# Performance work log

Hardware: AMD Instinct MI355X
Metric: run time of the kernel (lower is better)

## Reference

```python
import jax, jax.numpy as jnp
import numpy as np

NUM_HEADS = 16
WINDOW = 256  # window_size: each query i attends to keys [max(0, i-W+1), i]


def setup_inputs() -> dict:
    key = jax.random.key(0)
    k1, k2, k3, k4, k5 = jax.random.split(key, 5)
    B, S, D = 2, 4096, 1024
    scale = 0.02
    return {
        "x": jax.random.normal(k1, (B, S, D), dtype=jnp.float32),
        "wq": jax.random.normal(k2, (D, D), dtype=jnp.float32) * scale,
        "wk": jax.random.normal(k3, (D, D), dtype=jnp.float32) * scale,
        "wv": jax.random.normal(k4, (D, D), dtype=jnp.float32) * scale,
        "wo": jax.random.normal(k5, (D, D), dtype=jnp.float32) * scale,
    }


def _sliding_window_attn(x, wq, wk, wv, wo):
    B, S, D = x.shape
    H, W = NUM_HEADS, WINDOW
    Dh = D // H
    nb = S // W  # number of query blocks (S assumed divisible by W)

    def proj(w):
        # nn.Linear: y = x @ w.T ; -> [B, H, nb, W, Dh]
        y = (x @ w.T).reshape(B, nb, W, H, Dh)
        return y.transpose(0, 3, 1, 2, 4)

    q = proj(wq)
    k = proj(wk)
    v = proj(wv)

    # Each query block j attends to key blocks j-1 and j (banded causal window).
    zpad = jnp.zeros((B, H, 1, W, Dh), dtype=x.dtype)
    kpad = jnp.concatenate([zpad, k], axis=2)  # [B,H,nb+1,W,Dh]
    vpad = jnp.concatenate([zpad, v], axis=2)
    k2 = jnp.concatenate([kpad[:, :, :-1], kpad[:, :, 1:]], axis=3)  # [B,H,nb,2W,Dh]
    v2 = jnp.concatenate([vpad[:, :, :-1], vpad[:, :, 1:]], axis=3)

    scores = jnp.einsum("bhjqd,bhjkd->bhjqk", q, k2) / jnp.sqrt(
        jnp.asarray(Dh, dtype=x.dtype)
    )  # [B,H,nb,W,2W]

    # Mask: query global pos i = j*W + qi; key global pos kp = (j-1)*W + ki.
    # Valid iff i-W+1 <= kp <= i  <=>  qi+1 <= ki <= qi+W ; and kp >= 0.
    qi = jnp.arange(W)[:, None]          # [W,1]
    ki = jnp.arange(2 * W)[None, :]      # [1,2W]
    band = (ki >= qi + 1) & (ki <= qi + W)                      # [W,2W]
    kpos_ok = (jnp.arange(nb)[:, None, None] - 1) * W + ki[None] >= 0  # [nb,1,2W]
    mask = band[None] & kpos_ok          # [nb,W,2W]

    neg = jnp.finfo(scores.dtype).min
    scores = jnp.where(mask[None, None], scores, neg)
    attn = jax.nn.softmax(scores, axis=-1)

    out = jnp.einsum("bhjqk,bhjkd->bhjqd", attn, v2)  # [B,H,nb,W,Dh]
    out = out.transpose(0, 2, 3, 1, 4).reshape(B, S, D)
    return out @ wo.T


def reference(x, wq, wk, wv, wo):
    return _sliding_window_attn(x, wq, wk, wv, wo)
```

## Files before the change

kernel.cpp:

```cpp
#include <hip/hip_runtime.h>

#define S_LEN 4096
#define DMODEL 1024
#define NH 16
#define DH 64
#define WIN 256
#define NQKV 3072

typedef __attribute__((ext_vector_type(8))) short short8;
typedef __attribute__((ext_vector_type(4))) short sh4;
typedef __attribute__((ext_vector_type(4))) float floatx4;

__device__ __forceinline__ ushort f2bf(float f) {
    union { float f; unsigned int i; } x;
    x.f = f;
    unsigned int r = x.i + 0x7FFFu + ((x.i >> 16) & 1u);
    return (ushort)(r >> 16);
}

__global__ __launch_bounds__(256) void cvt_all(const float* __restrict__ x,
                                               const float* __restrict__ wq,
                                               const float* __restrict__ wk,
                                               const float* __restrict__ wv,
                                               const float* __restrict__ wo,
                                               ushort* __restrict__ xb,
                                               ushort* __restrict__ W3b,
                                               ushort* __restrict__ wob,
                                               int nx8, int nw8) {
    int i = blockIdx.x * 256 + threadIdx.x;
    const float* src;
    ushort* dst;
    if (i < nx8) {
        src = x + (size_t)i * 8;            dst = xb + (size_t)i * 8;
    } else {
        int j = i - nx8;
        int which = j / nw8, r = j - which * nw8;
        if (which >= 4) return;
        const float* w4[4] = {wq, wk, wv, wo};
        src = w4[which] + (size_t)r * 8;
        dst = (which == 3 ? wob : W3b + (size_t)which * nw8 * 8) + (size_t)r * 8;
    }
    floatx4 f0 = *(const floatx4*)src;
    floatx4 f1 = *(const floatx4*)(src + 4);
    short8 v;
#pragma unroll
    for (int e = 0; e < 4; ++e) v[e] = (short)f2bf(f0[e]);
#pragma unroll
    for (int e = 0; e < 4; ++e) v[4 + e] = (short)f2bf(f1[e]);
    *(short8*)dst = v;
}

#define GLOAD16(src, dst)                                                     \
    __builtin_amdgcn_global_load_lds(                                         \
        (const __attribute__((address_space(1))) void*)(src),                 \
        (__attribute__((address_space(3))) void*)(dst), 16, 0, 0)

template <bool OUTF32>
__global__ __launch_bounds__(256, 2) void gemm128(const ushort* __restrict__ A,
                                                  const ushort* __restrict__ W,
                                                  void* __restrict__ Cout,
                                                  int M, int N, int K) {
    __shared__ __align__(16) ushort As[128 * 64];
    __shared__ __align__(16) ushort Ws[256 * 64];

    const int tid = threadIdx.x;
    const int w = tid >> 6, l = tid & 63;

    int bx, by;
    {
        const int nbx = gridDim.x, nby = gridDim.y;
        if ((nby & 7) == 0) {
            const int lin = blockIdx.y * nbx + blockIdx.x;
            const int rpb = nby >> 3;
            const int xcd = lin & 7, idx = lin >> 3;
            bx = idx / rpb;
            by = xcd * rpb + (idx - bx * rpb);
        } else {
            bx = blockIdx.x;
            by = blockIdx.y;
        }
    }
    const int bm0 = by * 128, bn0 = bx * 256;
    const int wm = (w >> 1) * 64, wn = (w & 1) * 128;
    const int lm = l & 15, quad = l >> 4;

    floatx4 acc[4][8] = {};

    int arow[4], acol[4];
#pragma unroll
    for (int p = 0; p < 4; ++p) {
        int c = p * 256 + tid;
        arow[p] = c >> 3;
        acol[p] = (((c & 7) ^ (arow[p] & 7))) * 8;
    }
    int wrow[8], wcol[8];
#pragma unroll
    for (int p = 0; p < 8; ++p) {
        int c = p * 256 + tid;
        wrow[p] = c >> 3;
        wcol[p] = (((c & 7) ^ (wrow[p] & 7))) * 8;
    }

    for (int k0 = 0; k0 < K; k0 += 64) {
#pragma unroll
        for (int p = 0; p < 4; ++p)
            GLOAD16(A + (size_t)(bm0 + arow[p]) * K + k0 + acol[p],
                    As + p * 2048 + tid * 8);
#pragma unroll
        for (int p = 0; p < 8; ++p)
            GLOAD16(W + (size_t)(bn0 + wrow[p]) * K + k0 + wcol[p],
                    Ws + p * 2048 + tid * 8);
        __syncthreads();

#pragma unroll
        for (int kk = 0; kk < 2; ++kk) {
            const int sseg = ((kk * 4 + quad) ^ (lm & 7)) * 8;
            short8 af[4], wf[8];
#pragma unroll
            for (int mi = 0; mi < 4; ++mi)
                af[mi] = *(const short8*)&As[(wm + mi * 16 + lm) * 64 + sseg];
#pragma unroll
            for (int ni = 0; ni < 8; ++ni)
                wf[ni] = *(const short8*)&Ws[(wn + ni * 16 + lm) * 64 + sseg];
#pragma unroll
            for (int mi = 0; mi < 4; ++mi)
#pragma unroll
                for (int ni = 0; ni < 8; ++ni)
                    acc[mi][ni] = __builtin_amdgcn_mfma_f32_16x16x32_bf16(
                        af[mi], wf[ni], acc[mi][ni], 0, 0, 0);
        }
        __syncthreads();
    }

#pragma unroll
    for (int mi = 0; mi < 4; ++mi)
#pragma unroll
        for (int ni = 0; ni < 8; ++ni)
#pragma unroll
            for (int r = 0; r < 4; ++r) {
                int row = bm0 + wm + mi * 16 + quad * 4 + r;
                int col = bn0 + wn + ni * 16 + lm;
                if constexpr (OUTF32)
                    ((float*)Cout)[(size_t)row * N + col] = acc[mi][ni][r];
                else
                    ((ushort*)Cout)[(size_t)row * N + col] = f2bf(acc[mi][ni][r]);
            }
}

#define KSP 72
#define VTP 136
#define PSP 40

__global__ __launch_bounds__(256) void swattn_mfma(const ushort* __restrict__ QKV,
                                                   ushort* __restrict__ O) {
    __shared__ __align__(16) ushort Ks[128 * KSP];
    __shared__ __align__(16) ushort Vt[64 * VTP];
    __shared__ __align__(16) ushort Ps[2][4 * 64 * PSP];
    __shared__ __align__(16) float lW[256];

    const int j = blockIdx.x, h = blockIdx.y, b = blockIdx.z;
    const int tid = threadIdx.x;
    const int w = tid >> 6, l = tid & 63;
    const int quad = l >> 4, lc = l & 15;

    const size_t base = (size_t)b * S_LEN * NQKV + (size_t)h * DH;
    const ushort* Qp = QKV + base;
    const ushort* Kp = QKV + base + DMODEL;
    const ushort* Vp = QKV + base + 2 * DMODEL;

    short8 qf[4][2];
#pragma unroll
    for (int nq = 0; nq < 4; ++nq)
#pragma unroll
        for (int kk = 0; kk < 2; ++kk)
            qf[nq][kk] = *(const short8*)(Qp +
                (size_t)(j * 256 + w * 64 + nq * 16 + lc) * NQKV + kk * 32 + quad * 8);

    floatx4 o[4][4] = {};
    float lsum[4] = {0.f, 0.f, 0.f, 0.f};

    const float sscale = 0.18033688011112042f;
    const float M0 = 2.0f;
    const int qlo = w * 64, qhi = w * 64 + 63;

    int skey[4], sseg[4];
#pragma unroll
    for (int i = 0; i < 4; ++i) {
        int cc = i * 256 + tid;
        skey[i] = cc >> 3;
        sseg[i] = cc & 7;
    }

    short8 kreg[4], vreg[4];
    const int c0 = (j == 0) ? 2 : 0;
    {
        const int kg0 = (j - 1) * 256 + c0 * 128;
#pragma unroll
        for (int i = 0; i < 4; ++i) {
            kreg[i] = *(const short8*)(Kp + (size_t)(kg0 + skey[i]) * NQKV + sseg[i] * 8);
            vreg[i] = *(const short8*)(Vp + (size_t)(kg0 + skey[i]) * NQKV + sseg[i] * 8);
        }
    }

    for (int c = c0; c < 4; ++c) {
        __syncthreads();
#pragma unroll
        for (int i = 0; i < 4; ++i) {
            *(short8*)&Ks[skey[i] * KSP + sseg[i] * 8] = kreg[i];
#pragma unroll
            for (int e = 0; e < 8; ++e)
                Vt[(e * 8 + sseg[i]) * VTP + skey[i]] = (ushort)vreg[i][e];
        }
        __syncthreads();

        if (c < 3) {
            const int kg0n = (j - 1) * 256 + (c + 1) * 128;
#pragma unroll
            for (int i = 0; i < 4; ++i) {
                kreg[i] = *(const short8*)(Kp + (size_t)(kg0n + skey[i]) * NQKV + sseg[i] * 8);
                vreg[i] = *(const short8*)(Vp + (size_t)(kg0n + skey[i]) * NQKV + sseg[i] * 8);
            }
        }

        const int krel0 = c * 128 - 256;
#pragma unroll
        for (int g = 0; g < 4; ++g) {
            const int k0 = krel0 + g * 32;
            if (k0 > qhi || k0 + 31 < qlo - 255) continue;
            ushort* Pw = &Ps[g & 1][w * 64 * PSP];

            floatx4 st[2][4];
            const floatx4 zero = {};
#pragma unroll
            for (int kt = 0; kt < 2; ++kt) {
                short8 kf0 = *(const short8*)&Ks[(g * 32 + kt * 16 + lc) * KSP + quad * 8];
                short8 kf1 = *(const short8*)&Ks[(g * 32 + kt * 16 + lc) * KSP + 32 + quad * 8];
#pragma unroll
                for (int nq = 0; nq < 4; ++nq) {
                    int kmin = k0 + kt * 16, qmin = qlo + nq * 16;
                    if (kmin > qmin + 15 || kmin + 270 < qmin) {
                        st[kt][nq] = zero;
                        continue;
                    }
                    st[kt][nq] = __builtin_amdgcn_mfma_f32_16x16x32_bf16(kf0, qf[nq][0], zero, 0, 0, 0);
                    st[kt][nq] = __builtin_amdgcn_mfma_f32_16x16x32_bf16(kf1, qf[nq][1], st[kt][nq], 0, 0, 0);
                }
            }
#pragma unroll
            for (int kt = 0; kt < 2; ++kt)
#pragma unroll
                for (int nq = 0; nq < 4; ++nq) {
                    sh4 pv;
                    int kmin = k0 + kt * 16, qmin = qlo + nq * 16;
                    if (kmin > qmin + 15 || kmin + 270 < qmin) {
                        pv[0] = pv[1] = pv[2] = pv[3] = 0;
                    } else if (kmin + 15 <= qmin && kmin + 240 >= qmin) {
#pragma unroll
                        for (int r = 0; r < 4; ++r) {
                            float p = exp2f(st[kt][nq][r] * sscale - M0);
                            lsum[nq] += p;
                            pv[r] = (short)f2bf(p);
                        }
                    } else {
#pragma unroll
                        for (int r = 0; r < 4; ++r) {
                            int krel = kmin + quad * 4 + r;
                            int qrel = qmin + lc;
                            bool valid = (krel <= qrel) && (krel + 255 >= qrel);
                            float p = valid ? exp2f(st[kt][nq][r] * sscale - M0) : 0.f;
                            lsum[nq] += p;
                            pv[r] = (short)f2bf(p);
                        }
                    }
                    *(sh4*)&Pw[(nq * 16 + lc) * PSP + kt * 16 + quad * 4] = pv;
                }
            __threadfence_block();

            short8 vf[4];
#pragma unroll
            for (int nd = 0; nd < 4; ++nd) {
                int prow = (lc & 7) * 8 + nd * 2 + (lc >> 3);
                vf[nd] = *(const short8*)&Vt[prow * VTP + g * 32 + quad * 8];
            }
#pragma unroll
            for (int mq = 0; mq < 4; ++mq) {
                int qmin = qlo + mq * 16;
                if (k0 > qmin + 15 || k0 + 286 < qmin) continue;
                short8 pf = *(const short8*)&Pw[(mq * 16 + lc) * PSP + quad * 8];
#pragma unroll
                for (int nd = 0; nd < 4; ++nd)
                    o[mq][nd] = __builtin_amdgcn_mfma_f32_16x16x32_bf16(pf, vf[nd], o[mq][nd], 0, 0, 0);
            }
        }
    }

#pragma unroll
    for (int nq = 0; nq < 4; ++nq) {
        lsum[nq] += __shfl_xor(lsum[nq], 16);
        lsum[nq] += __shfl_xor(lsum[nq], 32);
    }
    if (l < 16) {
#pragma unroll
        for (int nq = 0; nq < 4; ++nq) lW[w * 64 + nq * 16 + l] = lsum[nq];
    }
    __threadfence_block();
#pragma unroll
    for (int mq = 0; mq < 4; ++mq) {
        floatx4 lv = *(const floatx4*)&lW[w * 64 + mq * 16 + quad * 4];
#pragma unroll
        for (int r = 0; r < 4; ++r) {
            float inv = 1.f / lv[r];
            int token = j * 256 + w * 64 + mq * 16 + quad * 4 + r;
#pragma unroll
            for (int nd = 0; nd < 4; ++nd)
                O[(size_t)b * S_LEN * DMODEL + (size_t)token * DMODEL + h * DH + nd * 16 + lc] =
                    f2bf(o[mq][nd][r] * inv);
        }
    }
}

extern "C" void kernel_launch(void* const* d_in, const int* in_sizes, int n_in,
                              void* d_out, int out_size, void* d_ws, size_t ws_size,
                              hipStream_t stream) {
    const float* x  = (const float*)d_in[0];
    const float* wq = (const float*)d_in[1];
    const float* wk = (const float*)d_in[2];
    const float* wv = (const float*)d_in[3];
    const float* wo = (const float*)d_in[4];
    float* out = (float*)d_out;

    const int D = DMODEL;
    const int M = in_sizes[0] / D;
    const int Bb = M / S_LEN;

    ushort* xb   = (ushort*)d_ws;
    ushort* W3b  = xb + (size_t)M * D;
    ushort* wob  = W3b + (size_t)NQKV * D;
    ushort* QKVb = wob + (size_t)D * D;
    ushort* Ob   = xb;

    const int nx8 = M * D / 8, nw8 = D * D / 8;
    const int ntot = nx8 + 4 * nw8;
    cvt_all<<<dim3((ntot + 255) / 256), dim3(256), 0, stream>>>(
        x, wq, wk, wv, wo, xb, W3b, wob, nx8, nw8);

    gemm128<false><<<dim3(NQKV / 256, M / 128), dim3(256), 0, stream>>>(
        xb, W3b, QKVb, M, NQKV, D);

    swattn_mfma<<<dim3(S_LEN / WIN, NH, Bb), dim3(256), 0, stream>>>(QKVb, Ob);

    gemm128<true><<<dim3(D / 256, M / 128), dim3(256), 0, stream>>>(
        Ob, wob, out, M, D, D);
}
```

Before: 226.1 us.

## Keep softmax probabilities in registers as MFMA operand, permute V layout to match

Drops the per-wave LDS staging buffer for the probability tile: the exp results stay in the score accumulators and are packed to bf16 with v_cvt_pk_bf16_f32, then fed straight into the PV MFMA as the A operand. To make the register layout of the transposed score fragment line up with the K dimension of the PV MFMA, the key columns of the transposed V tile in LDS are permuted when stored. This removes LDS writes, reads and a block fence per 32-key group and frees shared memory, but relies on the custom permutation exactly matching the MFMA register layout and uses inline asm with truncation-vs-rounding differences.

```diff
diff --git a/kernel.cpp b/kernel.cpp
--- a/kernel.cpp
+++ b/kernel.cpp
@@ -149,13 +149,11 @@
 
 #define KSP 72
 #define VTP 136
-#define PSP 40
 
 __global__ __launch_bounds__(256) void swattn_mfma(const ushort* __restrict__ QKV,
                                                    ushort* __restrict__ O) {
     __shared__ __align__(16) ushort Ks[128 * KSP];
     __shared__ __align__(16) ushort Vt[64 * VTP];
-    __shared__ __align__(16) ushort Ps[2][4 * 64 * PSP];
     __shared__ __align__(16) float lW[256];
 
     const int j = blockIdx.x, h = blockIdx.y, b = blockIdx.z;
@@ -183,12 +181,14 @@
     const float M0 = 2.0f;
     const int qlo = w * 64, qhi = w * 64 + 63;
 
-    int skey[4], sseg[4];
+    int skey[4], sseg[4], svcol[4];
 #pragma unroll
     for (int i = 0; i < 4; ++i) {
         int cc = i * 256 + tid;
         skey[i] = cc >> 3;
         sseg[i] = cc & 7;
+        int k = skey[i];
+        svcol[i] = (k & 96) + ((k >> 2) & 3) * 8 + ((k >> 4) & 1) * 4 + (k & 3);
     }
 
     short8 kreg[4], vreg[4];
@@ -209,7 +209,7 @@
             *(short8*)&Ks[skey[i] * KSP + sseg[i] * 8] = kreg[i];
 #pragma unroll
             for (int e = 0; e < 8; ++e)
-                Vt[(e * 8 + sseg[i]) * VTP + skey[i]] = (ushort)vreg[i][e];
+                Vt[(e * 8 + sseg[i]) * VTP + svcol[i]] = (ushort)vreg[i][e];
         }
         __syncthreads();
 
@@ -227,7 +227,6 @@
         for (int g = 0; g < 4; ++g) {
             const int k0 = krel0 + g * 32;
             if (k0 > qhi || k0 + 31 < qlo - 255) continue;
-            ushort* Pw = &Ps[g & 1][w * 64 * PSP];
 
             floatx4 st[2][4];
             const floatx4 zero = {};
@@ -250,16 +249,15 @@
             for (int kt = 0; kt < 2; ++kt)
 #pragma unroll
                 for (int nq = 0; nq < 4; ++nq) {
-                    sh4 pv;
                     int kmin = k0 + kt * 16, qmin = qlo + nq * 16;
                     if (kmin > qmin + 15 || kmin + 270 < qmin) {
-                        pv[0] = pv[1] = pv[2] = pv[3] = 0;
+                        st[kt][nq] = zero;
                     } else if (kmin + 15 <= qmin && kmin + 240 >= qmin) {
 #pragma unroll
                         for (int r = 0; r < 4; ++r) {
                             float p = exp2f(st[kt][nq][r] * sscale - M0);
                             lsum[nq] += p;
-                            pv[r] = (short)f2bf(p);
+                            st[kt][nq][r] = p;
                         }
                     } else {
 #pragma unroll
@@ -269,12 +267,10 @@
                             bool valid = (krel <= qrel) && (krel + 255 >= qrel);
                             float p = valid ? exp2f(st[kt][nq][r] * sscale - M0) : 0.f;
                             lsum[nq] += p;
-                            pv[r] = (short)f2bf(p);
+                            st[kt][nq][r] = p;
                         }
                     }
-                    *(sh4*)&Pw[(nq * 16 + lc) * PSP + kt * 16 + quad * 4] = pv;
                 }
-            __threadfence_block();
 
             short8 vf[4];
 #pragma unroll
@@ -286,10 +282,18 @@
             for (int mq = 0; mq < 4; ++mq) {
                 int qmin = qlo + mq * 16;
                 if (k0 > qmin + 15 || k0 + 286 < qmin) continue;
-                short8 pf = *(const short8*)&Pw[(mq * 16 + lc) * PSP + quad * 8];
+                union { unsigned int u[4]; short8 s; } pk;
+                asm("v_cvt_pk_bf16_f32 %0, %1, %2"
+                    : "=v"(pk.u[0]) : "v"(st[0][mq][0]), "v"(st[0][mq][1]));
+                asm("v_cvt_pk_bf16_f32 %0, %1, %2"
+                    : "=v"(pk.u[1]) : "v"(st[0][mq][2]), "v"(st[0][mq][3]));
+                asm("v_cvt_pk_bf16_f32 %0, %1, %2"
+                    : "=v"(pk.u[2]) : "v"(st[1][mq][0]), "v"(st[1][mq][1]));
+                asm("v_cvt_pk_bf16_f32 %0, %1, %2"
+                    : "=v"(pk.u[3]) : "v"(st[1][mq][2]), "v"(st[1][mq][3]));
 #pragma unroll
                 for (int nd = 0; nd < 4; ++nd)
-                    o[mq][nd] = __builtin_amdgcn_mfma_f32_16x16x32_bf16(pf, vf[nd], o[mq][nd], 0, 0, 0);
+                    o[mq][nd] = __builtin_amdgcn_mfma_f32_16x16x32_bf16(pk.s, vf[nd], o[mq][nd], 0, 0, 0);
             }
         }
     }
```

After: 221.1 us. 1.02x faster.
